# Optimization experiments

Measured on AMD Instinct MI355X. Metric: run time of the kernel, lower is better.

## Reference

```python
import jax, jax.numpy as jnp
import numpy as np

NUM_HEADS = 16
HEAD_DIM = 64  # latent_dim // num_heads = 1024 // 16


def setup_inputs() -> dict:
    key = jax.random.key(0)
    k1, k2, k3, k4 = jax.random.split(key, 4)
    B, S, C = 4, 2048, 1024
    x = jax.random.normal(k1, (B, S, C), dtype=jnp.float32)
    # torch nn.Linear weight layout: [out_features, in_features]
    W_qkv = jax.random.normal(k2, (2 * 1024 + C, C), dtype=jnp.float32) * (C ** -0.5)
    W_out = jax.random.normal(k3, (C, C), dtype=jnp.float32) * (C ** -0.5)
    b_out = jax.random.normal(k4, (C,), dtype=jnp.float32) * 0.01
    return {"x": x, "W_qkv": W_qkv, "W_out": W_out, "b_out": b_out}


def reference(x, W_qkv, W_out, b_out):
    B, S, C = x.shape
    H, CH = NUM_HEADS, HEAD_DIM
    qkv = jnp.einsum('bsc,oc->bso', x, W_qkv)          # [B, S, 2*latent + C]
    qkv = qkv.reshape(B, S, H, -1)                      # per-head: [CH, CH, C//H]
    q = qkv[..., :CH]
    k = qkv[..., CH:2 * CH]
    v = qkv[..., 2 * CH:]
    energy = jnp.einsum('bqhc,bkhc->bhqk', q, k)        # full score matrix
    scale = jnp.asarray(C, x.dtype) ** 0.5              # note: original scales by sqrt(C), not sqrt(head_dim)
    attn = jax.nn.softmax(energy / scale, axis=-1)
    out = jnp.einsum('bhqk,bkhc->bqhc', attn, v).reshape(B, S, -1)
    out = jnp.einsum('bsc,oc->bso', out, W_out) + b_out
    return out + x
```

## Files before the change

kernel.cpp:

```cpp
#include <hip/hip_runtime.h>
#include <hip/hip_bf16.h>
#include <stdint.h>

#define BB 4
#define SS 2048
#define CC 1024
#define HH 16
#define DD 64
#define MTOT (BB*SS)
#define NQKV 3072

typedef __attribute__((ext_vector_type(8))) short short8;
typedef __attribute__((ext_vector_type(4))) float f32x4;

#define MFMA16(A,B,C) __builtin_amdgcn_mfma_f32_16x16x32_bf16((A),(B),(C),0,0,0)

__device__ __forceinline__ ushort f2bf(float f) {
  uint32_t u = __builtin_bit_cast(uint32_t, f);
  u += 0x7FFFu + ((u >> 16) & 1u);
  return (ushort)(u >> 16);
}

__device__ __forceinline__ unsigned pk2bf(float a, float b) {
  return (unsigned)f2bf(a) | ((unsigned)f2bf(b) << 16);
}

__device__ __forceinline__ float hw_exp2(float x) {
  float r;
  asm("v_exp_f32 %0, %1" : "=v"(r) : "v"(x));
  return r;
}

__global__ void cvt_kernel(const float* __restrict__ src, ushort* __restrict__ dst, int n4) {
  int stride = gridDim.x * blockDim.x;
  for (int i = blockIdx.x * blockDim.x + threadIdx.x; i < n4; i += stride) {
    float4 v = reinterpret_cast<const float4*>(src)[i];
    ushort4 o;
    o.x = f2bf(v.x); o.y = f2bf(v.y); o.z = f2bf(v.z); o.w = f2bf(v.w);
    reinterpret_cast<ushort4*>(dst)[i] = o;
  }
}

__device__ __forceinline__ void stage8k(const ushort* g0, int ldk, ushort* lds, int wave, int lane) {
  #pragma unroll
  for (int r = 0; r < 2; ++r) {
    int chunk = r * 256 + wave * 64 + lane;
    int row = chunk >> 2;
    int co  = (chunk & 3) * 8;
    const ushort* src = g0 + (size_t)row * ldk + co;
    ushort* dst = lds + (size_t)(r * 256 + wave * 64) * 8;
    __builtin_amdgcn_global_load_lds(
        (const __attribute__((address_space(1))) uint32_t*)src,
        (__attribute__((address_space(3))) uint32_t*)dst, 16, 0, 0);
  }
}

__device__ __forceinline__ void gemm_loop(const ushort* __restrict__ A, const ushort* __restrict__ Bw,
                                          int m0, int n0, ushort* As, ushort* Bs, f32x4 acc[4][4]) {
  const int lane = threadIdx.x & 63, wave = threadIdx.x >> 6;
  const int g = lane >> 4, q = lane & 15;
  const int wm = (wave >> 1) * 64, wn = (wave & 1) * 64;
  const ushort* Ag = A + (size_t)m0 * 1024;
  const ushort* Bg = Bw + (size_t)n0 * 1024;
  #pragma unroll 1
  for (int k0 = 0; k0 < 1024; k0 += 32) {
    stage8k(Ag + k0, 1024, As, wave, lane);
    stage8k(Bg + k0, 1024, Bs, wave, lane);
    __syncthreads();
    short8 af[4], bf[4];
    #pragma unroll
    for (int i = 0; i < 4; ++i)
      af[i] = *(const short8*)(As + (wm + i * 16 + q) * 32 + g * 8);
    #pragma unroll
    for (int j = 0; j < 4; ++j)
      bf[j] = *(const short8*)(Bs + (wn + j * 16 + q) * 32 + g * 8);
    #pragma unroll
    for (int i = 0; i < 4; ++i)
      #pragma unroll
      for (int j = 0; j < 4; ++j)
        acc[i][j] = MFMA16(af[i], bf[j], acc[i][j]);
    __syncthreads();
  }
}

__global__ __launch_bounds__(256) void gemm_qkv(const ushort* __restrict__ xb, const ushort* __restrict__ wqkv,
                                                ushort* __restrict__ qfbuf, ushort* __restrict__ kfbuf,
                                                ushort* __restrict__ vfbuf) {
  __shared__ ushort As[128 * 32], Bs[128 * 32];
  const int m0 = blockIdx.x * 128, n0 = blockIdx.y * 128;
  f32x4 acc[4][4];
  #pragma unroll
  for (int i = 0; i < 4; ++i)
    #pragma unroll
    for (int j = 0; j < 4; ++j) acc[i][j] = f32x4{0.f, 0.f, 0.f, 0.f};
  gemm_loop(xb, wqkv, m0, n0, As, Bs, acc);

  const int lane = threadIdx.x & 63, wave = threadIdx.x >> 6;
  const int g = lane >> 4, q = lane & 15;
  const int wm = (wave >> 1) * 64, wn = (wave & 1) * 64;
  #pragma unroll
  for (int j = 0; j < 4; ++j) {
    int n = n0 + wn + j * 16 + q;
    int h = n / 192;
    int rem = n - h * 192;
    int which = rem >> 6;
    int c = rem & 63;
    float scl = (which == 0) ? 0.045084222f : 1.0f;
    #pragma unroll
    for (int i = 0; i < 4; ++i) {
      int mb = m0 + wm + i * 16 + g * 4;
      #pragma unroll
      for (int r = 0; r < 4; ++r) {
        int m = mb + r;
        int b = m >> 11, s = m & 2047;
        int bh = b * 16 + h;
        ushort val = f2bf(acc[i][j][r] * scl);
        if (which < 2) {
          int jt = s >> 4, c0 = c >> 5, lane2 = ((c >> 3) & 3) * 16 + (s & 15), e = c & 7;
          size_t idx = ((((size_t)bh * 128 + jt) * 2 + c0) * 64 + lane2) * 8 + e;
          if (which == 0) qfbuf[idx] = val; else kfbuf[idx] = val;
        } else {
          int jc = s >> 5, gg = (s >> 3) & 3, e = s & 7, ct = c >> 4, qq = c & 15;
          size_t idx = ((((size_t)bh * 64 + jc) * 4 + ct) * 64 + gg * 16 + qq) * 8 + e;
          vfbuf[idx] = val;
        }
      }
    }
  }
}

__global__ __launch_bounds__(256) void attn_kernel(const ushort* __restrict__ QF, const ushort* __restrict__ KF,
                                                   const ushort* __restrict__ VF, ushort* __restrict__ aout) {
  __shared__ ushort Ps[4][2][16 * 72];
  const int bh = blockIdx.x, qb = blockIdx.y;
  const int lane = threadIdx.x & 63, wave = threadIdx.x >> 6;
  const int g = lane >> 4, q = lane & 15;
  const int qt0 = (qb * 4 + wave) * 2;
  const f32x4 zed = {0.f, 0.f, 0.f, 0.f};

  const ushort* Qb = QF + (size_t)bh * 131072 + lane * 8;
  const ushort* Kb = KF + (size_t)bh * 131072 + lane * 8;
  const ushort* Vb = VF + (size_t)bh * 131072 + lane * 8;

  short8 onesf;
  #pragma unroll
  for (int e = 0; e < 8; ++e) onesf[e] = (short)0x3F80;

  short8 qf[2][2];
  #pragma unroll
  for (int t = 0; t < 2; ++t)
    #pragma unroll
    for (int c0 = 0; c0 < 2; ++c0)
      qf[t][c0] = *(const short8*)(Qb + ((size_t)(qt0 + t) * 2 + c0) * 512);

  f32x4 oa[2][4], la[2];
  #pragma unroll
  for (int t = 0; t < 2; ++t) {
    la[t] = zed;
    #pragma unroll
    for (int ct = 0; ct < 4; ++ct) oa[t][ct] = zed;
  }

  #pragma unroll 1
  for (int j0 = 0; j0 < SS; j0 += 64) {
    const int jt0 = j0 >> 4, jc0 = j0 >> 5;
    short8 kf[4][2], vf[2][4];
    #pragma unroll
    for (int jt = 0; jt < 4; ++jt)
      #pragma unroll
      for (int c0 = 0; c0 < 2; ++c0)
        kf[jt][c0] = *(const short8*)(Kb + ((size_t)(jt0 + jt) * 2 + c0) * 512);
    #pragma unroll
    for (int jc = 0; jc < 2; ++jc)
      #pragma unroll
      for (int ct = 0; ct < 4; ++ct)
        vf[jc][ct] = *(const short8*)(Vb + ((size_t)(jc0 + jc) * 4 + ct) * 512);

    #pragma unroll
    for (int t = 0; t < 2; ++t) {
      f32x4 sa[4];
      __builtin_amdgcn_s_setprio(1);
      #pragma unroll
      for (int jt = 0; jt < 4; ++jt) {
        sa[jt] = MFMA16(kf[jt][0], qf[t][0], zed);
        sa[jt] = MFMA16(kf[jt][1], qf[t][1], sa[jt]);
      }
      __builtin_amdgcn_s_setprio(0);
      float p[4][4];
      #pragma unroll
      for (int jt = 0; jt < 4; ++jt)
        #pragma unroll
        for (int r = 0; r < 4; ++r) p[jt][r] = hw_exp2(sa[jt][r]);
      ushort* pw = Ps[wave][t];
      #pragma unroll
      for (int jt = 0; jt < 4; ++jt) {
        uint2 w;
        w.x = pk2bf(p[jt][0], p[jt][1]);
        w.y = pk2bf(p[jt][2], p[jt][3]);
        *reinterpret_cast<uint2*>(pw + q * 72 + jt * 16 + 4 * g) = w;
      }
      #pragma unroll
      for (int jc = 0; jc < 2; ++jc) {
        short8 pa = *reinterpret_cast<const short8*>(pw + q * 72 + jc * 32 + g * 8);
        __builtin_amdgcn_s_setprio(1);
        #pragma unroll
        for (int ct = 0; ct < 4; ++ct)
          oa[t][ct] = MFMA16(pa, vf[jc][ct], oa[t][ct]);
        la[t] = MFMA16(pa, onesf, la[t]);
        __builtin_amdgcn_s_setprio(0);
      }
    }
  }

  const int b = bh >> 4, h = bh & 15;
  #pragma unroll
  for (int t = 0; t < 2; ++t) {
    float inv[4];
    #pragma unroll
    for (int r = 0; r < 4; ++r) inv[r] = 1.0f / la[t][r];
    #pragma unroll
    for (int ct = 0; ct < 4; ++ct) {
      size_t rowb = (size_t)b * SS + (qt0 + t) * 16 + 4 * g;
      int col = h * DD + ct * 16 + q;
      aout[(rowb + 0) * CC + col] = f2bf(oa[t][ct][0] * inv[0]);
      aout[(rowb + 1) * CC + col] = f2bf(oa[t][ct][1] * inv[1]);
      aout[(rowb + 2) * CC + col] = f2bf(oa[t][ct][2] * inv[2]);
      aout[(rowb + 3) * CC + col] = f2bf(oa[t][ct][3] * inv[3]);
    }
  }
}

__global__ __launch_bounds__(256) void gemm_out(const ushort* __restrict__ ab, const ushort* __restrict__ wout,
                                                const float* __restrict__ x, const float* __restrict__ bias,
                                                float* __restrict__ out) {
  __shared__ ushort As[128 * 32], Bs[128 * 32];
  const int m0 = blockIdx.x * 128, n0 = blockIdx.y * 128;
  f32x4 acc[4][4];
  #pragma unroll
  for (int i = 0; i < 4; ++i)
    #pragma unroll
    for (int j = 0; j < 4; ++j) acc[i][j] = f32x4{0.f, 0.f, 0.f, 0.f};
  gemm_loop(ab, wout, m0, n0, As, Bs, acc);

  const int lane = threadIdx.x & 63, wave = threadIdx.x >> 6;
  const int g = lane >> 4, q = lane & 15;
  const int wm = (wave >> 1) * 64, wn = (wave & 1) * 64;
  #pragma unroll
  for (int j = 0; j < 4; ++j) {
    int n = n0 + wn + j * 16 + q;
    float bj = bias[n];
    #pragma unroll
    for (int i = 0; i < 4; ++i) {
      int mb = m0 + wm + i * 16 + g * 4;
      #pragma unroll
      for (int r = 0; r < 4; ++r) {
        size_t m = (size_t)(mb + r);
        out[m * CC + n] = acc[i][j][r] + bj + x[m * CC + n];
      }
    }
  }
}

extern "C" void kernel_launch(void* const* d_in, const int* in_sizes, int n_in,
                              void* d_out, int out_size, void* d_ws, size_t ws_size,
                              hipStream_t stream) {
  const float* x    = (const float*)d_in[0];
  const float* wqkv = (const float*)d_in[1];
  const float* wout = (const float*)d_in[2];
  const float* bias = (const float*)d_in[3];
  float* out = (float*)d_out;

  ushort* xb    = (ushort*)d_ws;
  ushort* wqkvb = xb + (size_t)8 * 1024 * 1024;
  ushort* woutb = wqkvb + (size_t)3 * 1024 * 1024;
  ushort* qfbuf = woutb + (size_t)1024 * 1024;
  ushort* kfbuf = qfbuf + (size_t)8 * 1024 * 1024;
  ushort* vfbuf = kfbuf + (size_t)8 * 1024 * 1024;
  ushort* aout  = vfbuf + (size_t)8 * 1024 * 1024;

  hipLaunchKernelGGL(cvt_kernel, dim3(2048), dim3(256), 0, stream, x, xb, 8 * 1024 * 1024 / 4);
  hipLaunchKernelGGL(cvt_kernel, dim3(1536), dim3(256), 0, stream, wqkv, wqkvb, 3 * 1024 * 1024 / 4);
  hipLaunchKernelGGL(cvt_kernel, dim3(512), dim3(256), 0, stream, wout, woutb, 1024 * 1024 / 4);

  hipLaunchKernelGGL(gemm_qkv, dim3(MTOT / 128, NQKV / 128), dim3(256), 0, stream,
                     xb, wqkvb, qfbuf, kfbuf, vfbuf);
  hipLaunchKernelGGL(attn_kernel, dim3(BB * HH, SS / 128), dim3(256), 0, stream,
                     qfbuf, kfbuf, vfbuf, aout);
  hipLaunchKernelGGL(gemm_out, dim3(MTOT / 128, CC / 128), dim3(256), 0, stream,
                     aout, woutb, x, bias, out);
}
```

Before: 233.3 us.

## Double-buffer K/V register fragments and use hardware packed bf16 conversion

Restructures the attention inner loop into a two-stage ping-pong over K/V register fragments, so the global loads for the next 64-key block are issued before the current block's MFMA and softmax work. This hides load latency behind compute. Separately, P is now converted to bf16 with the v_cvt_pk_bf16_f32 instruction instead of manual integer rounding. The cost is higher VGPR pressure, which could lower occupancy or cause spills.

```diff
diff --git a/kernel.cpp b/kernel.cpp
--- a/kernel.cpp
+++ b/kernel.cpp
@@ -21,8 +21,10 @@
   return (ushort)(u >> 16);
 }
 
-__device__ __forceinline__ unsigned pk2bf(float a, float b) {
-  return (unsigned)f2bf(a) | ((unsigned)f2bf(b) << 16);
+__device__ __forceinline__ unsigned cvtpk(float lo, float hi) {
+  unsigned r;
+  asm("v_cvt_pk_bf16_f32 %0, %1, %2" : "=v"(r) : "v"(lo), "v"(hi));
+  return r;
 }
 
 __device__ __forceinline__ float hw_exp2(float x) {
@@ -129,6 +131,43 @@
   }
 }
 
+
+__device__ __forceinline__ void attn_step(const short8 kf[4][2], const short8 vf[2][4],
+                                          const short8 qf[2][2], const short8 onesf,
+                                          f32x4 oa[2][4], f32x4 la[2],
+                                          ushort* pw0, int g, int q) {
+  const f32x4 zed = {0.f, 0.f, 0.f, 0.f};
+  #pragma unroll
+  for (int t = 0; t < 2; ++t) {
+    f32x4 sa[4];
+    __builtin_amdgcn_s_setprio(1);
+    #pragma unroll
+    for (int jt = 0; jt < 4; ++jt) {
+      sa[jt] = MFMA16(kf[jt][0], qf[t][0], zed);
+      sa[jt] = MFMA16(kf[jt][1], qf[t][1], sa[jt]);
+    }
+    __builtin_amdgcn_s_setprio(0);
+    ushort* pw = pw0 + t * 1152;
+    #pragma unroll
+    for (int jt = 0; jt < 4; ++jt) {
+      uint2 w;
+      w.x = cvtpk(hw_exp2(sa[jt][0]), hw_exp2(sa[jt][1]));
+      w.y = cvtpk(hw_exp2(sa[jt][2]), hw_exp2(sa[jt][3]));
+      *reinterpret_cast<uint2*>(pw + q * 72 + jt * 16 + 4 * g) = w;
+    }
+    #pragma unroll
+    for (int jc = 0; jc < 2; ++jc) {
+      short8 pa = *reinterpret_cast<const short8*>(pw + q * 72 + jc * 32 + g * 8);
+      __builtin_amdgcn_s_setprio(1);
+      #pragma unroll
+      for (int ct = 0; ct < 4; ++ct)
+        oa[t][ct] = MFMA16(pa, vf[jc][ct], oa[t][ct]);
+      la[t] = MFMA16(pa, onesf, la[t]);
+      __builtin_amdgcn_s_setprio(0);
+    }
+  }
+}
+
 __global__ __launch_bounds__(256) void attn_kernel(const ushort* __restrict__ QF, const ushort* __restrict__ KF,
                                                    const ushort* __restrict__ VF, ushort* __restrict__ aout) {
   __shared__ ushort Ps[4][2][16 * 72];
@@ -139,8 +178,9 @@
   const f32x4 zed = {0.f, 0.f, 0.f, 0.f};
 
   const ushort* Qb = QF + (size_t)bh * 131072 + lane * 8;
-  const ushort* Kb = KF + (size_t)bh * 131072 + lane * 8;
-  const ushort* Vb = VF + (size_t)bh * 131072 + lane * 8;
+  const ushort* Kp = KF + (size_t)bh * 131072 + lane * 8;
+  const ushort* Vp = VF + (size_t)bh * 131072 + lane * 8;
+  ushort* pw0 = Ps[wave][0];
 
   short8 onesf;
   #pragma unroll
@@ -161,55 +201,44 @@
     for (int ct = 0; ct < 4; ++ct) oa[t][ct] = zed;
   }
 
+  short8 kfA[4][2], kfB[4][2], vfA[2][4], vfB[2][4];
+  #pragma unroll
+  for (int jt = 0; jt < 4; ++jt)
+    #pragma unroll
+    for (int c0 = 0; c0 < 2; ++c0)
+      kfA[jt][c0] = *(const short8*)(Kp + ((size_t)jt * 2 + c0) * 512);
+
   #pragma unroll 1
-  for (int j0 = 0; j0 < SS; j0 += 64) {
-    const int jt0 = j0 >> 4, jc0 = j0 >> 5;
-    short8 kf[4][2], vf[2][4];
+  for (int i = 0; i < 32; i += 2) {
+    #pragma unroll
+    for (int jc = 0; jc < 2; ++jc)
+      #pragma unroll
+      for (int ct = 0; ct < 4; ++ct)
+        vfA[jc][ct] = *(const short8*)(Vp + ((size_t)jc * 4 + ct) * 512);
     #pragma unroll
     for (int jt = 0; jt < 4; ++jt)
       #pragma unroll
       for (int c0 = 0; c0 < 2; ++c0)
-        kf[jt][c0] = *(const short8*)(Kb + ((size_t)(jt0 + jt) * 2 + c0) * 512);
+        kfB[jt][c0] = *(const short8*)(Kp + 4096 + ((size_t)jt * 2 + c0) * 512);
+
+    attn_step(kfA, vfA, qf, onesf, oa, la, pw0, g, q);
+
     #pragma unroll
     for (int jc = 0; jc < 2; ++jc)
       #pragma unroll
       for (int ct = 0; ct < 4; ++ct)
-        vf[jc][ct] = *(const short8*)(Vb + ((size_t)(jc0 + jc) * 4 + ct) * 512);
-
-    #pragma unroll
-    for (int t = 0; t < 2; ++t) {
-      f32x4 sa[4];
-      __builtin_amdgcn_s_setprio(1);
-      #pragma unroll
-      for (int jt = 0; jt < 4; ++jt) {
-        sa[jt] = MFMA16(kf[jt][0], qf[t][0], zed);
-        sa[jt] = MFMA16(kf[jt][1], qf[t][1], sa[jt]);
-      }
-      __builtin_amdgcn_s_setprio(0);
-      float p[4][4];
+        vfB[jc][ct] = *(const short8*)(Vp + 4096 + ((size_t)jc * 4 + ct) * 512);
+    if (i + 2 < 32) {
       #pragma unroll
       for (int jt = 0; jt < 4; ++jt)
         #pragma unroll
-        for (int r = 0; r < 4; ++r) p[jt][r] = hw_exp2(sa[jt][r]);
-      ushort* pw = Ps[wave][t];
-      #pragma unroll
-      for (int jt = 0; jt < 4; ++jt) {
-        uint2 w;
-        w.x = pk2bf(p[jt][0], p[jt][1]);
-        w.y = pk2bf(p[jt][2], p[jt][3]);
-        *reinterpret_cast<uint2*>(pw + q * 72 + jt * 16 + 4 * g) = w;
-      }
-      #pragma unroll
-      for (int jc = 0; jc < 2; ++jc) {
-        short8 pa = *reinterpret_cast<const short8*>(pw + q * 72 + jc * 32 + g * 8);
-        __builtin_amdgcn_s_setprio(1);
-        #pragma unroll
-        for (int ct = 0; ct < 4; ++ct)
-          oa[t][ct] = MFMA16(pa, vf[jc][ct], oa[t][ct]);
-        la[t] = MFMA16(pa, onesf, la[t]);
-        __builtin_amdgcn_s_setprio(0);
-      }
-    }
+        for (int c0 = 0; c0 < 2; ++c0)
+          kfA[jt][c0] = *(const short8*)(Kp + 8192 + ((size_t)jt * 2 + c0) * 512);
+    }
+
+    attn_step(kfB, vfB, qf, onesf, oa, la, pw0, g, q);
+
+    Kp += 8192; Vp += 8192;
   }
 
   const int b = bh >> 4, h = bh & 15;
```

After: 222.5 us. 4.6% less time.
